# Optimization experiments

Hardware: AMD Instinct MI355X
Metric: run time of the kernel (lower is better)

Reference implementation:

```python
import jax, jax.numpy as jnp
import numpy as np

B, N, C = 4, 2048, 1024
H = 16
HD = C // H
SCALE = HD ** -0.5


def setup_inputs() -> dict:
    key = jax.random.key(0)
    k1, k2, k3, k4 = jax.random.split(key, 4)
    x = jax.random.normal(k1, (B, N, C), dtype=jnp.float32)
    w_qkv = jax.random.normal(k2, (3 * C, C), dtype=jnp.float32) * (C ** -0.5)
    w_proj = jax.random.normal(k3, (C, C), dtype=jnp.float32) * (C ** -0.5)
    b_proj = jax.random.normal(k4, (C,), dtype=jnp.float32) * 0.01
    return {"x": x, "w_qkv": w_qkv, "w_proj": w_proj, "b_proj": b_proj}


def reference(x, w_qkv, w_proj, b_proj):
    qkv = jnp.einsum('bnc,dc->bnd', x, w_qkv)
    qkv = qkv.reshape(B, N, 3, H, HD).transpose(2, 0, 3, 1, 4)
    q, k, v = qkv[0], qkv[1], qkv[2]
    # scaled dot-product attention with explicit softmax (dropout p=0 -> identity)
    attn = jnp.einsum('bhqd,bhkd->bhqk', q, k) * SCALE
    attn = jax.nn.softmax(attn, axis=-1)
    out = jnp.einsum('bhqk,bhkd->bhqd', attn, v)
    out = out.transpose(0, 2, 1, 3).reshape(B, N, C)
    # output projection
    return jnp.einsum('bnc,dc->bnd', out, w_proj) + b_proj
```

## Files before the change

### kernel.cpp

```cpp
#include <hip/hip_runtime.h>

typedef unsigned short u16;
typedef unsigned int u32;
typedef __bf16 bf16x8 __attribute__((ext_vector_type(8)));
typedef __bf16 bf16x4 __attribute__((ext_vector_type(4)));
typedef short s16x4 __attribute__((ext_vector_type(4)));
typedef float f32x4 __attribute__((ext_vector_type(4)));
typedef float f32x16 __attribute__((ext_vector_type(16)));
typedef unsigned int u32x2 __attribute__((ext_vector_type(2)));
typedef unsigned int u32x4 __attribute__((ext_vector_type(4)));

struct __align__(8) u16x4 { u16 x, y, z, w; };

__device__ __forceinline__ void async_copy16(const void* g, void* l) {
  __builtin_amdgcn_global_load_lds(
      (__attribute__((address_space(1))) void*)g,
      (__attribute__((address_space(3))) void*)l, 16, 0, 0);
}

__device__ __forceinline__ u16 f2bf(float f) {
  unsigned u = __builtin_bit_cast(unsigned, f);
  u = (u + 0x7FFFu + ((u >> 16) & 1u)) >> 16;
  return (u16)u;
}
__device__ __forceinline__ float bf2f(u16 h) {
  unsigned u = ((unsigned)h) << 16;
  return __builtin_bit_cast(float, u);
}

__device__ __forceinline__ float fast_exp2(float x) {
  return __builtin_amdgcn_exp2f(x);
}
__device__ __forceinline__ float fast_rcp(float x) {
  return __builtin_amdgcn_rcpf(x);
}

__device__ __forceinline__ f32x4 mfma32(bf16x8 a, bf16x8 b, f32x4 c) {
  return __builtin_amdgcn_mfma_f32_16x16x32_bf16(a, b, c, 0, 0, 0);
}

__device__ __forceinline__ u32 cvt_pk_bf16(float lo, float hi) {
  u32 r;
  asm("v_cvt_pk_bf16_f32 %0, %1, %2" : "=v"(r) : "v"(lo), "v"(hi));
  return r;
}

#define CEXP 0.18033688011112042f

__global__ void detect_mode(const u32* __restrict__ probe, int* __restrict__ flag) {
  __shared__ int cnt[256];
  int t = threadIdx.x;
  int c = 0;
#pragma unroll
  for (int j = 0; j < 16; ++j) {
    u32 v = probe[t + j * 256];
    unsigned e = (v >> 7) & 0xFFu;
    c += (e >= 100u && e <= 130u) ? 1 : 0;
  }
  cnt[t] = c;
  __syncthreads();
  for (int s = 128; s > 0; s >>= 1) {
    if (t < s) cnt[t] += cnt[t + s];
    __syncthreads();
  }
  if (t == 0) *flag = (cnt[0] * 2 > 4096) ? 1 : 0;
}

__global__ void convert_in(const void* __restrict__ src, u16* __restrict__ dst,
                           const int* __restrict__ flag, int n) {
  int mode = *flag;
  int i = (blockIdx.x * blockDim.x + threadIdx.x) * 8;
  if (i >= n) return;
  if (mode == 1) {
    *(uint4*)(dst + i) = *(const uint4*)((const u16*)src + i);
  } else {
    const float* s = (const float*)src;
    float4 a = *(const float4*)(s + i);
    float4 b = *(const float4*)(s + i + 4);
    uint4 o;
    o.x = (u32)f2bf(a.x) | ((u32)f2bf(a.y) << 16);
    o.y = (u32)f2bf(a.z) | ((u32)f2bf(a.w) << 16);
    o.z = (u32)f2bf(b.x) | ((u32)f2bf(b.y) << 16);
    o.w = (u32)f2bf(b.z) | ((u32)f2bf(b.w) << 16);
    *(uint4*)(dst + i) = o;
  }
}

template<int NJ>
__global__ __launch_bounds__(512, 2) void gemm_bt(
    const u16* __restrict__ A, const u16* __restrict__ Bm,
    u16* __restrict__ C, u16* __restrict__ vT, const u16* __restrict__ bias,
    float* __restrict__ outF, const int* __restrict__ flagp,
    int K, int ldc)
{
  __shared__ __align__(16) char lds[65536 + NJ * 16384];

  const int t = threadIdx.x;
  const int lane = t & 63, wave = t >> 6;
  const int quad = lane >> 4, l16 = lane & 15;
  const int wn = wave & 3, wm = wave >> 2;

  const int nwg = gridDim.x * gridDim.y;
  int bid = blockIdx.y * gridDim.x + blockIdx.x;
  bid = (bid & 7) * (nwg >> 3) + (bid >> 3);
  const int rowbase = (bid / gridDim.x) * 256;
  const int colbase = (bid % gridDim.x) * (NJ * 64);

  const int srow = t >> 3;
  const int scol = ((t & 7) << 4) ^ ((srow & 7) << 4);
  const int wlds = wave << 10;

  const u16* Arow = A + (size_t)(rowbase + srow) * K + (scol >> 1);
  const u16* Brow = Bm + (size_t)(colbase + srow) * K + (scol >> 1);

  auto stageA = [&](int kb_, int buf_) {
#pragma unroll
    for (int q = 0; q < 4; ++q)
      async_copy16(Arow + (size_t)kb_ * 64 + (size_t)q * 64 * K,
                   lds + buf_ * 32768 + q * 8192 + wlds);
  };
  auto stageB = [&](int kb_, int buf_) {
#pragma unroll
    for (int q = 0; q < NJ; ++q)
      async_copy16(Brow + (size_t)kb_ * 64 + (size_t)q * 64 * K,
                   lds + 65536 + buf_ * (NJ * 8192) + q * 8192 + wlds);
  };

  f32x4 acc[8][NJ] = {};

  const int swzl = (l16 & 7) << 4;
  const int c0 = (quad * 16) ^ swzl;
  const int c1 = (64 + quad * 16) ^ swzl;
  const char* Ard = lds + (size_t)(wm * 128 + l16) * 128;
  const char* Brd = lds + 65536 + (size_t)(wn * (NJ * 16) + l16) * 128;

  stageA(0, 0); stageB(0, 0);
  stageA(1, 1); stageB(1, 1);
  if constexpr (NJ == 3) asm volatile("s_waitcnt vmcnt(7)" ::: "memory");
  else                   asm volatile("s_waitcnt vmcnt(6)" ::: "memory");
  __builtin_amdgcn_s_barrier();

  const int nkb = K >> 6;
  for (int kb = 0; kb < nkb; ++kb) {
    const int cur = kb & 1;
    const char* Ab = Ard + cur * 32768;
    const char* Bb = Brd + cur * (NJ * 8192);

    if constexpr (NJ == 2) {
      bf16x8 aR[4][2], bR[2][2];
#pragma unroll
      for (int i = 0; i < 4; ++i) {
        aR[i][0] = *(const bf16x8*)(Ab + i * 2048 + c0);
        aR[i][1] = *(const bf16x8*)(Ab + i * 2048 + c1);
      }
#pragma unroll
      for (int j = 0; j < 2; ++j) {
        bR[j][0] = *(const bf16x8*)(Bb + j * 2048 + c0);
        bR[j][1] = *(const bf16x8*)(Bb + j * 2048 + c1);
      }
      __builtin_amdgcn_s_barrier();
      __builtin_amdgcn_s_setprio(1);
#pragma unroll
      for (int i = 0; i < 4; ++i)
#pragma unroll
        for (int j = 0; j < 2; ++j) {
          acc[i][j] = mfma32(aR[i][0], bR[j][0], acc[i][j]);
          acc[i][j] = mfma32(aR[i][1], bR[j][1], acc[i][j]);
        }
      __builtin_amdgcn_s_setprio(0);
      __builtin_amdgcn_s_barrier();
      if (kb + 2 < nkb) stageB(kb + 2, cur);

#pragma unroll
      for (int i = 0; i < 4; ++i) {
        aR[i][0] = *(const bf16x8*)(Ab + 8192 + i * 2048 + c0);
        aR[i][1] = *(const bf16x8*)(Ab + 8192 + i * 2048 + c1);
      }
      __builtin_amdgcn_s_barrier();
      __builtin_amdgcn_s_setprio(1);
#pragma unroll
      for (int i = 0; i < 4; ++i)
#pragma unroll
        for (int j = 0; j < 2; ++j) {
          acc[4 + i][j] = mfma32(aR[i][0], bR[j][0], acc[4 + i][j]);
          acc[4 + i][j] = mfma32(aR[i][1], bR[j][1], acc[4 + i][j]);
        }
      __builtin_amdgcn_s_setprio(0);
      __builtin_amdgcn_s_barrier();
    } else {
      bf16x8 aR[4], bR[NJ][2];

#pragma unroll
      for (int i = 0; i < 4; ++i) aR[i] = *(const bf16x8*)(Ab + i * 2048 + c0);
#pragma unroll
      for (int j = 0; j < NJ; ++j) {
        bR[j][0] = *(const bf16x8*)(Bb + j * 2048 + c0);
        bR[j][1] = *(const bf16x8*)(Bb + j * 2048 + c1);
      }
      __builtin_amdgcn_s_barrier();
      __builtin_amdgcn_s_setprio(1);
#pragma unroll
      for (int i = 0; i < 4; ++i)
#pragma unroll
        for (int j = 0; j < NJ; ++j)
          acc[i][j] = mfma32(aR[i], bR[j][0], acc[i][j]);
      __builtin_amdgcn_s_setprio(0);
      __builtin_amdgcn_s_barrier();

#pragma unroll
      for (int i = 0; i < 4; ++i) aR[i] = *(const bf16x8*)(Ab + i * 2048 + c1);
      __builtin_amdgcn_s_barrier();
      __builtin_amdgcn_s_setprio(1);
#pragma unroll
      for (int i = 0; i < 4; ++i)
#pragma unroll
        for (int j = 0; j < NJ; ++j)
          acc[i][j] = mfma32(aR[i], bR[j][1], acc[i][j]);
      __builtin_amdgcn_s_setprio(0);
      __builtin_amdgcn_s_barrier();
      if (kb + 2 < nkb) stageB(kb + 2, cur);

#pragma unroll
      for (int i = 0; i < 4; ++i) aR[i] = *(const bf16x8*)(Ab + 8192 + i * 2048 + c1);
      __builtin_amdgcn_s_barrier();
      __builtin_amdgcn_s_setprio(1);
#pragma unroll
      for (int i = 0; i < 4; ++i)
#pragma unroll
        for (int j = 0; j < NJ; ++j)
          acc[4 + i][j] = mfma32(aR[i], bR[j][1], acc[4 + i][j]);
      __builtin_amdgcn_s_setprio(0);
      __builtin_amdgcn_s_barrier();

#pragma unroll
      for (int i = 0; i < 4; ++i) aR[i] = *(const bf16x8*)(Ab + 8192 + i * 2048 + c0);
      __builtin_amdgcn_s_barrier();
      __builtin_amdgcn_s_setprio(1);
#pragma unroll
      for (int i = 0; i < 4; ++i)
#pragma unroll
        for (int j = 0; j < NJ; ++j)
          acc[4 + i][j] = mfma32(aR[i], bR[j][0], acc[4 + i][j]);
      __builtin_amdgcn_s_setprio(0);
      __builtin_amdgcn_s_barrier();
    }

    if (kb + 2 < nkb) {
      stageA(kb + 2, cur);
      if constexpr (NJ == 3) asm volatile("s_waitcnt vmcnt(7)" ::: "memory");
      else                   asm volatile("s_waitcnt vmcnt(6)" ::: "memory");
      __builtin_amdgcn_s_barrier();
    } else if (kb + 1 < nkb) {
      asm volatile("s_waitcnt vmcnt(0)" ::: "memory");
      __builtin_amdgcn_s_barrier();
    }
  }

  const bool f32out = (flagp != nullptr) && (*flagp == 0);
#pragma unroll
  for (int nj = 0; nj < NJ; ++nj) {
    int cg = colbase + wn * (NJ * 16) + nj * 16 + l16;
    if (vT != nullptr && cg >= 2048) {
#pragma unroll
      for (int mi = 0; mi < 8; ++mi) {
        int rg = rowbase + wm * 128 + mi * 16 + quad * 4;
        int b = rg >> 11, n = rg & 2047;
        size_t idx = ((size_t)(b * 1024 + (cg - 2048))) * 2048 + n;
        u16x4 pk;
        pk.x = f2bf(acc[mi][nj][0]); pk.y = f2bf(acc[mi][nj][1]);
        pk.z = f2bf(acc[mi][nj][2]); pk.w = f2bf(acc[mi][nj][3]);
        *(u16x4*)(vT + idx) = pk;
      }
    } else {
      const float scl = (vT != nullptr && cg < 1024) ? CEXP : 1.0f;
      float bv = bias ? bf2f(bias[cg]) : 0.0f;
#pragma unroll
      for (int mi = 0; mi < 8; ++mi) {
#pragma unroll
        for (int r = 0; r < 4; ++r) {
          int rg = rowbase + wm * 128 + mi * 16 + quad * 4 + r;
          float val = acc[mi][nj][r] * scl + bv;
          if (f32out) outF[(size_t)rg * ldc + cg] = val;
          else        C[(size_t)rg * ldc + cg] = f2bf(val);
        }
      }
    }
  }
}

__global__ __launch_bounds__(256, 4) void attn_fwd(
    const u16* __restrict__ qk, const u16* __restrict__ vT, u16* __restrict__ outp)
{
  __shared__ __align__(16) char sm[32768];

  const int t = threadIdx.x;
  const int lane = t & 63, wave = t >> 6;
  const int l31 = lane & 31, h32 = lane >> 5;
  const int bh = blockIdx.x, b = bh >> 4, h = bh & 15;
  const int qtile = blockIdx.y;
  const size_t row0 = (size_t)b * 2048;
  const int qb = qtile * 128 + wave * 32;

  bf16x8 qf[4];
  {
    const u16* qp = qk + (row0 + qb + l31) * 2048 + h * 64 + h32 * 8;
#pragma unroll
    for (int s = 0; s < 4; ++s)
      qf[s] = *(const bf16x8*)(qp + s * 16);
  }

  const u16* Kg[2]; const u16* Vg[2]; unsigned loff[2];
#pragma unroll
  for (int q = 0; q < 2; ++q) {
    int si = q * 256 + t;
    int srow = si >> 3;
    int scolb = ((si & 7) << 4) ^ ((srow & 7) << 4);
    Kg[q] = qk + (row0 + srow) * 2048 + 1024 + h * 64 + (scolb >> 1);
    Vg[q] = vT + ((size_t)(b * 1024 + h * 64 + srow)) * 2048 + (scolb >> 1);
    loff[q] = q * 4096 + wave * 1024;
  }

#pragma unroll
  for (int q = 0; q < 2; ++q) {
    async_copy16(Kg[q], sm + loff[q]);
    async_copy16(Vg[q], sm + 16384 + loff[q]);
  }

  const int swz = (lane & 7) << 4;
  int cswz[4];
#pragma unroll
  for (int s = 0; s < 4; ++s) cswz[s] = (s * 32 + h32 * 16) ^ swz;
  const int rowb = l31 * 128;

  u32x4 onev; onev.x = 0x3F803F80u; onev.y = 0x3F803F80u;
  onev.z = 0x3F803F80u; onev.w = 0x3F803F80u;
  const bf16x8 ones = __builtin_bit_cast(bf16x8, onev);

  f32x16 o2[2] = {};
  f32x16 o3 = {};

  for (int kb = 0; kb < 32; ++kb) {
    const int cur = kb & 1, nxt = cur ^ 1;
    __builtin_amdgcn_s_barrier();
    if (kb < 31) {
#pragma unroll
      for (int q = 0; q < 2; ++q) {
        async_copy16(Kg[q] + (size_t)(kb + 1) * 64 * 2048, sm + nxt * 8192 + loff[q]);
        async_copy16(Vg[q] + (kb + 1) * 64, sm + 16384 + nxt * 8192 + loff[q]);
      }
      asm volatile("s_waitcnt vmcnt(4)" ::: "memory");
    } else {
      asm volatile("s_waitcnt vmcnt(0)" ::: "memory");
    }
    __builtin_amdgcn_s_barrier();

    const char* Kb = sm + cur * 8192;
    const char* Vb = sm + 16384 + cur * 8192;

#pragma unroll
    for (int kh = 0; kh < 2; ++kh) {
      f32x16 s2 = {};
      __builtin_amdgcn_s_setprio(1);
#pragma unroll
      for (int s = 0; s < 4; ++s) {
        bf16x8 kf = *(const bf16x8*)(Kb + kh * 4096 + rowb + cswz[s]);
        s2 = __builtin_amdgcn_mfma_f32_32x32x16_bf16(kf, qf[s], s2, 0, 0, 0);
      }
      __builtin_amdgcn_s_setprio(0);

      u32 u[8];
#pragma unroll
      for (int w = 0; w < 8; ++w) {
        float p0 = fast_exp2(s2[2 * w]);
        float p1 = fast_exp2(s2[2 * w + 1]);
        u[w] = cvt_pk_bf16(p0, p1);
      }

      u32x2 r02 = __builtin_amdgcn_permlane32_swap(u[0], u[2], false, false);
      u32x2 r13 = __builtin_amdgcn_permlane32_swap(u[1], u[3], false, false);
      u32x2 r46 = __builtin_amdgcn_permlane32_swap(u[4], u[6], false, false);
      u32x2 r57 = __builtin_amdgcn_permlane32_swap(u[5], u[7], false, false);
      u32x4 fa0v; fa0v.x = r02.x; fa0v.y = r13.x; fa0v.z = r02.y; fa0v.w = r13.y;
      u32x4 fa1v; fa1v.x = r46.x; fa1v.y = r57.x; fa1v.z = r46.y; fa1v.w = r57.y;
      bf16x8 fa0 = __builtin_bit_cast(bf16x8, fa0v);
      bf16x8 fa1 = __builtin_bit_cast(bf16x8, fa1v);

      __builtin_amdgcn_s_setprio(1);
#pragma unroll
      for (int eb = 0; eb < 2; ++eb) {
        bf16x8 v0 = *(const bf16x8*)(Vb + eb * 4096 + rowb + cswz[kh * 2 + 0]);
        o2[eb] = __builtin_amdgcn_mfma_f32_32x32x16_bf16(fa0, v0, o2[eb], 0, 0, 0);
        bf16x8 v1 = *(const bf16x8*)(Vb + eb * 4096 + rowb + cswz[kh * 2 + 1]);
        o2[eb] = __builtin_amdgcn_mfma_f32_32x32x16_bf16(fa1, v1, o2[eb], 0, 0, 0);
      }
      o3 = __builtin_amdgcn_mfma_f32_32x32x16_bf16(fa0, ones, o3, 0, 0, 0);
      o3 = __builtin_amdgcn_mfma_f32_32x32x16_bf16(fa1, ones, o3, 0, 0, 0);
      __builtin_amdgcn_s_setprio(0);
    }
  }

#pragma unroll
  for (int r = 0; r < 16; ++r) {
    int qr = (r & 3) + 8 * (r >> 2) + 4 * h32;
    float iv = fast_rcp(o3[r]);
    size_t base = (row0 + qb + qr) * 1024 + h * 64 + l31;
    outp[base]      = f2bf(o2[0][r] * iv);
    outp[base + 32] = f2bf(o2[1][r] * iv);
  }
}

extern "C" void kernel_launch(void* const* d_in, const int* in_sizes, int n_in,
                              void* d_out, int out_size, void* d_ws, size_t ws_size,
                              hipStream_t stream) {
  (void)in_sizes; (void)n_in; (void)out_size; (void)ws_size;
  const void* x_in     = d_in[0];
  const void* wqkv_in  = d_in[1];
  const void* wproj_in = d_in[2];
  const void* bproj_in = d_in[3];

  u16* qkbuf  = (u16*)d_ws;
  u16* vT     = qkbuf + 16777216;
  u16* xb     = vT + 8388608;
  u16* wqkvb  = xb + 8388608;
  int* flag   = (int*)(wqkvb + 3145728);
  u16* attn   = xb;
  u16* wprojb = vT;
  u16* bprojb = vT + 1048576;

  detect_mode<<<1, 256, 0, stream>>>((const u32*)wqkv_in, flag);
  convert_in<<<4096, 256, 0, stream>>>(x_in, xb, flag, 8388608);
  convert_in<<<1536, 256, 0, stream>>>(wqkv_in, wqkvb, flag, 3145728);

  gemm_bt<3><<<dim3(16, 32), 512, 0, stream>>>(xb, wqkvb, qkbuf, vT, nullptr,
                                               nullptr, nullptr, 1024, 2048);
  attn_fwd<<<dim3(64, 16), 256, 0, stream>>>(qkbuf, vT, attn);

  convert_in<<<512, 256, 0, stream>>>(wproj_in, wprojb, flag, 1048576);
  convert_in<<<1, 256, 0, stream>>>(bproj_in, bprojb, flag, 1024);

  gemm_bt<2><<<dim3(8, 32), 512, 0, stream>>>(attn, wprojb, (u16*)d_out, nullptr,
                                              bprojb, (float*)d_out, flag, 1024, 1024);
}
```

Measured before the change: 275.2 us.

## Spread GEMM prefetch across MFMA phases and widen attention blocks to 512 threads

In the NJ=3 GEMM path, the B-tile prefetch now issues earlier and the A-tile prefetch is split into two halves interleaved between MFMA phases, instead of being issued in one burst at the end of the iteration. Wait counts are adjusted to match. The attention kernel now uses 512-thread blocks covering 256 query rows, so each K/V tile in LDS is shared by twice as many waves and each thread issues one async copy per tile instead of two. The aim is better overlap of global loads with compute and fewer redundant K/V loads, at the cost of fewer, larger attention workgroups and tighter vmcnt bookkeeping.

Result: faster. 269.4 us (-2.1%).

```diff
diff --git a/kernel.cpp b/kernel.cpp
--- a/kernel.cpp
+++ b/kernel.cpp
@@ -113,6 +113,12 @@
   const u16* Arow = A + (size_t)(rowbase + srow) * K + (scol >> 1);
   const u16* Brow = Bm + (size_t)(colbase + srow) * K + (scol >> 1);
 
+  auto stageA2 = [&](int kb_, int buf_, int qa, int qb2) {
+    async_copy16(Arow + (size_t)kb_ * 64 + (size_t)qa * 64 * K,
+                 lds + buf_ * 32768 + qa * 8192 + wlds);
+    async_copy16(Arow + (size_t)kb_ * 64 + (size_t)qb2 * 64 * K,
+                 lds + buf_ * 32768 + qb2 * 8192 + wlds);
+  };
   auto stageA = [&](int kb_, int buf_) {
 #pragma unroll
     for (int q = 0; q < 4; ++q)
@@ -145,6 +151,7 @@
     const int cur = kb & 1;
     const char* Ab = Ard + cur * 32768;
     const char* Bb = Brd + cur * (NJ * 8192);
+    const bool pf = (kb + 2 < nkb);
 
     if constexpr (NJ == 2) {
       bf16x8 aR[4][2], bR[2][2];
@@ -169,7 +176,7 @@
         }
       __builtin_amdgcn_s_setprio(0);
       __builtin_amdgcn_s_barrier();
-      if (kb + 2 < nkb) stageB(kb + 2, cur);
+      if (pf) stageB(kb + 2, cur);
 
 #pragma unroll
       for (int i = 0; i < 4; ++i) {
@@ -187,6 +194,15 @@
         }
       __builtin_amdgcn_s_setprio(0);
       __builtin_amdgcn_s_barrier();
+
+      if (pf) {
+        stageA(kb + 2, cur);
+        asm volatile("s_waitcnt vmcnt(6)" ::: "memory");
+        __builtin_amdgcn_s_barrier();
+      } else if (kb + 1 < nkb) {
+        asm volatile("s_waitcnt vmcnt(0)" ::: "memory");
+        __builtin_amdgcn_s_barrier();
+      }
     } else {
       bf16x8 aR[4], bR[NJ][2];
 
@@ -206,6 +222,7 @@
           acc[i][j] = mfma32(aR[i], bR[j][0], acc[i][j]);
       __builtin_amdgcn_s_setprio(0);
       __builtin_amdgcn_s_barrier();
+      if (pf) stageB(kb + 2, cur);
 
 #pragma unroll
       for (int i = 0; i < 4; ++i) aR[i] = *(const bf16x8*)(Ab + i * 2048 + c1);
@@ -218,7 +235,7 @@
           acc[i][j] = mfma32(aR[i], bR[j][1], acc[i][j]);
       __builtin_amdgcn_s_setprio(0);
       __builtin_amdgcn_s_barrier();
-      if (kb + 2 < nkb) stageB(kb + 2, cur);
+      if (pf) stageA2(kb + 2, cur, 0, 2);
 
 #pragma unroll
       for (int i = 0; i < 4; ++i) aR[i] = *(const bf16x8*)(Ab + 8192 + i * 2048 + c1);
@@ -243,16 +260,15 @@
           acc[4 + i][j] = mfma32(aR[i], bR[j][0], acc[4 + i][j]);
       __builtin_amdgcn_s_setprio(0);
       __builtin_amdgcn_s_barrier();
-    }
-
-    if (kb + 2 < nkb) {
-      stageA(kb + 2, cur);
-      if constexpr (NJ == 3) asm volatile("s_waitcnt vmcnt(7)" ::: "memory");
-      else                   asm volatile("s_waitcnt vmcnt(6)" ::: "memory");
-      __builtin_amdgcn_s_barrier();
-    } else if (kb + 1 < nkb) {
-      asm volatile("s_waitcnt vmcnt(0)" ::: "memory");
-      __builtin_amdgcn_s_barrier();
+
+      if (pf) {
+        stageA2(kb + 2, cur, 1, 3);
+        asm volatile("s_waitcnt vmcnt(7)" ::: "memory");
+        __builtin_amdgcn_s_barrier();
+      } else if (kb + 1 < nkb) {
+        asm volatile("s_waitcnt vmcnt(0)" ::: "memory");
+        __builtin_amdgcn_s_barrier();
+      }
     }
   }
 
@@ -288,7 +304,7 @@
   }
 }
 
-__global__ __launch_bounds__(256, 4) void attn_fwd(
+__global__ __launch_bounds__(512, 2) void attn_fwd(
     const u16* __restrict__ qk, const u16* __restrict__ vT, u16* __restrict__ outp)
 {
   __shared__ __align__(16) char sm[32768];
@@ -299,7 +315,7 @@
   const int bh = blockIdx.x, b = bh >> 4, h = bh & 15;
   const int qtile = blockIdx.y;
   const size_t row0 = (size_t)b * 2048;
-  const int qb = qtile * 128 + wave * 32;
+  const int qb = qtile * 256 + wave * 32;
 
   bf16x8 qf[4];
   {
@@ -309,22 +325,14 @@
       qf[s] = *(const bf16x8*)(qp + s * 16);
   }
 
-  const u16* Kg[2]; const u16* Vg[2]; unsigned loff[2];
-#pragma unroll
-  for (int q = 0; q < 2; ++q) {
-    int si = q * 256 + t;
-    int srow = si >> 3;
-    int scolb = ((si & 7) << 4) ^ ((srow & 7) << 4);
-    Kg[q] = qk + (row0 + srow) * 2048 + 1024 + h * 64 + (scolb >> 1);
-    Vg[q] = vT + ((size_t)(b * 1024 + h * 64 + srow)) * 2048 + (scolb >> 1);
-    loff[q] = q * 4096 + wave * 1024;
-  }
-
-#pragma unroll
-  for (int q = 0; q < 2; ++q) {
-    async_copy16(Kg[q], sm + loff[q]);
-    async_copy16(Vg[q], sm + 16384 + loff[q]);
-  }
+  const int srow = t >> 3;
+  const int scolb = ((t & 7) << 4) ^ ((srow & 7) << 4);
+  const u16* Kg = qk + (row0 + srow) * 2048 + 1024 + h * 64 + (scolb >> 1);
+  const u16* Vg = vT + ((size_t)(b * 1024 + h * 64 + srow)) * 2048 + (scolb >> 1);
+  const unsigned loff = (unsigned)wave << 10;
+
+  async_copy16(Kg, sm + loff);
+  async_copy16(Vg, sm + 16384 + loff);
 
   const int swz = (lane & 7) << 4;
   int cswz[4];
@@ -343,12 +351,9 @@
     const int cur = kb & 1, nxt = cur ^ 1;
     __builtin_amdgcn_s_barrier();
     if (kb < 31) {
-#pragma unroll
-      for (int q = 0; q < 2; ++q) {
-        async_copy16(Kg[q] + (size_t)(kb + 1) * 64 * 2048, sm + nxt * 8192 + loff[q]);
-        async_copy16(Vg[q] + (kb + 1) * 64, sm + 16384 + nxt * 8192 + loff[q]);
-      }
-      asm volatile("s_waitcnt vmcnt(4)" ::: "memory");
+      async_copy16(Kg + (size_t)(kb + 1) * 64 * 2048, sm + nxt * 8192 + loff);
+      async_copy16(Vg + (kb + 1) * 64, sm + 16384 + nxt * 8192 + loff);
+      asm volatile("s_waitcnt vmcnt(2)" ::: "memory");
     } else {
       asm volatile("s_waitcnt vmcnt(0)" ::: "memory");
     }
@@ -433,7 +438,7 @@
 
   gemm_bt<3><<<dim3(16, 32), 512, 0, stream>>>(xb, wqkvb, qkbuf, vT, nullptr,
                                                nullptr, nullptr, 1024, 2048);
-  attn_fwd<<<dim3(64, 16), 256, 0, stream>>>(qkbuf, vT, attn);
+  attn_fwd<<<dim3(64, 8), 512, 0, stream>>>(qkbuf, vT, attn);
 
   convert_in<<<512, 256, 0, stream>>>(wproj_in, wprojb, flag, 1048576);
   convert_in<<<1, 256, 0, stream>>>(bproj_in, bprojb, flag, 1024);
```
